# Optimization experiments

Hardware: AMD Instinct MI355X
Metric: run time of the kernel (lower is better)

The kernel has to match this reference:

```python
import jax, jax.numpy as jnp
import numpy as np


def setup_inputs() -> dict:
    key = jax.random.key(0)
    k1, k2 = jax.random.split(key)
    inputs = jax.random.normal(k1, (4, 128, 64, 64), dtype=jnp.float32)
    # binary hole mask (1 = known background, 0 = hole), broadcast over channels
    mask = jnp.round(jax.random.uniform(k2, (4, 1, 64, 64), dtype=jnp.float32))
    return {"inputs": inputs, "mask": mask}


def reference(inputs, mask):
    # SFFA contextual attention with 1x1 dynamic kernels.
    # Note: in the original torch code the 1x1 conv with padding=1 produces
    # border scores that conv_transpose2d with padding=1 crops away exactly,
    # so the math reduces to per-pixel matmul + softmax + matmul.
    bz, nc, h, w = inputs.shape
    N = h * w
    background = inputs * mask                              # [b, c, h, w]
    # dynamic kernels: one nc-dim vector per background pixel (patch)
    K = background.reshape(bz, nc, N).transpose(0, 2, 1) + 1e-7   # [b, N, c]
    Kn = K / jnp.sqrt(jnp.sum(K * K, axis=2, keepdims=True))      # l2-normalized
    feat = inputs.reshape(bz, nc, N)                        # [b, c, N]
    scores = jnp.einsum('bpc,bcn->bpn', Kn, feat)           # [b, N(patch), N(pixel)]
    attn = jax.nn.softmax(scores, axis=1)                   # softmax over patches p
    agg = jnp.einsum('bpc,bpn->bcn', K, attn).reshape(bz, nc, h, w)
    return background + agg * (1.0 - mask)
```

## Files before the change

### kernel.cpp

```cpp
#include <hip/hip_runtime.h>
#include <hip/hip_bf16.h>

typedef __attribute__((ext_vector_type(8))) short bf16x8;
typedef __attribute__((ext_vector_type(4))) float f32x4;

#define NPIX 4096
#define NC   128
#define RS128 0.08838834764831845f
#define KSP  6

#define GL2LDS(g, l) __builtin_amdgcn_global_load_lds( \
    (const __attribute__((address_space(1))) void*)(g), \
    (__attribute__((address_space(3))) void*)(l), 16, 0, 0)

__global__ __launch_bounds__(1024) void sffa_prep(
    const float* __restrict__ x, const float* __restrict__ mask,
    ushort* __restrict__ KnW, ushort* __restrict__ QW, ushort* __restrict__ VtW,
    float* __restrict__ s0c, int* __restrict__ pixQ, int* __restrict__ cnts,
    float* __restrict__ out)
{
    __shared__ float xs[128][69];
    __shared__ float ms[64];
    __shared__ float rinv[64];
    __shared__ float ssum[64];
    __shared__ float2 part[16][64];
    __shared__ int se[64];
    __shared__ int bgn[64];
    __shared__ int tinfo[2];
    __shared__ int wredP[16], wredT[16];
    const int tid = threadIdx.x;
    const int b = blockIdx.x >> 6, nblk = blockIdx.x & 63;
    const int n0 = nblk * 64;
    const float* xb = x + (size_t)b * NC * NPIX;
    float* ob = out + (size_t)b * NC * NPIX;

    #pragma unroll
    for (int it = 0; it < 2; ++it) {
        int e4 = it * 1024 + tid;
        int c = e4 >> 4, n4 = (e4 & 15) * 4;
        float4 v = *(const float4*)(xb + (size_t)c * NPIX + n0 + n4);
        xs[c][n4+0] = v.x; xs[c][n4+1] = v.y; xs[c][n4+2] = v.z; xs[c][n4+3] = v.w;
        *(float4*)(ob + (size_t)c * NPIX + n0 + n4) = v;
    }
    if (tid < 16) {
        float4 mv = *(const float4*)(mask + (size_t)b * NPIX + n0 + tid * 4);
        ms[tid*4+0] = mv.x; ms[tid*4+1] = mv.y; ms[tid*4+2] = mv.z; ms[tid*4+3] = mv.w;
    }
    {
        const int lane = tid & 63, w = tid >> 6;
        float4 mv = *(const float4*)(mask + (size_t)b * NPIX + tid * 4);
        int f0 = mv.x < 0.5f ? 0x10000 : 1;
        int f1 = mv.y < 0.5f ? 0x10000 : 1;
        int f2 = mv.z < 0.5f ? 0x10000 : 1;
        int f3 = mv.w < 0.5f ? 0x10000 : 1;
        int p0 = tid * 4;
        int pre = 0, tot = f0 + f1 + f2 + f3;
        if (p0 + 0 < n0) pre += f0;
        if (p0 + 1 < n0) pre += f1;
        if (p0 + 2 < n0) pre += f2;
        if (p0 + 3 < n0) pre += f3;
        #pragma unroll
        for (int d = 1; d < 64; d <<= 1) {
            pre += __shfl_xor(pre, d);
            tot += __shfl_xor(tot, d);
        }
        if (lane == 0) { wredP[w] = pre; wredT[w] = tot; }
    }
    __syncthreads();
    if (tid < 64) {
        int vP = (tid < 16) ? wredP[tid] : 0;
        int vT = (tid < 16) ? wredT[tid] : 0;
        #pragma unroll
        for (int d = 1; d < 16; d <<= 1) {
            vP += __shfl_xor(vP, d);
            vT += __shfl_xor(vT, d);
        }
        int base  = __shfl(vP, 0);
        int total = __shfl(vT, 0);
        if (tid == 0 && nblk == 0) {
            cnts[b * 2]     = total & 0xffff;
            cnts[b * 2 + 1] = total >> 16;
        }
        int f = ms[tid] > 0.5f ? 1 : 0x10000;
        int s = f;
        #pragma unroll
        for (int d = 1; d < 64; d <<= 1) {
            int t = __shfl_up(s, d);
            if (tid >= d) s += t;
        }
        se[tid] = base + s - f;
    }
    __syncthreads();
    {
        int p = tid & 63, qd = tid >> 6;
        float m = ms[p];
        float s2 = 0.f, s1 = 0.f;
        #pragma unroll
        for (int i = 0; i < 8; ++i) {
            float xv = xs[qd*8 + i][p];
            float k = fmaf(xv, m, 1e-7f);
            s2 = fmaf(k, k, s2);
            s1 += xv;
        }
        part[qd][p] = make_float2(s2, s1);
    }
    __syncthreads();
    if (tid < 64) {
        float s2 = 0.f, s1 = 0.f;
        #pragma unroll
        for (int k = 0; k < 16; ++k) { float2 t = part[k][tid]; s2 += t.x; s1 += t.y; }
        rinv[tid] = rsqrtf(s2);
        ssum[tid] = s1 * RS128;
    }
    __syncthreads();
    #pragma unroll
    for (int it = 0; it < 4; ++it) {
        int e2 = it * 1024 + tid;
        int n = e2 >> 6, cp = (e2 & 63) * 2;
        int pe = se[n];
        float x0 = xs[cp][n], x1 = xs[cp+1][n];
        if (ms[n] > 0.5f) {
            int slot = pe & 0xffff;
            float k0 = x0 + 1e-7f, k1 = x1 + 1e-7f;
            float r = rinv[n];
            __hip_bfloat162 kn;
            kn.x = __float2bfloat16(k0 * r); kn.y = __float2bfloat16(k1 * r);
            *(__hip_bfloat162*)(KnW + ((size_t)b * NPIX + slot) * NC + cp) = kn;
        } else {
            int slot = pe >> 16;
            __hip_bfloat162 q;
            q.x = __float2bfloat16(x0); q.y = __float2bfloat16(x1);
            *(__hip_bfloat162*)(QW + ((size_t)b * NPIX + slot) * NC + cp) = q;
        }
    }
    if (tid < 64) {
        if (ms[tid] < 0.5f) {
            int slot = se[tid] >> 16;
            s0c [(size_t)b * NPIX + slot] = ssum[tid];
            pixQ[(size_t)b * NPIX + slot] = n0 + tid;
        } else {
            bgn[(se[tid] & 0xffff) - (se[0] & 0xffff)] = tid;
        }
    }
    if (tid == 0) {
        tinfo[0] = se[0] & 0xffff;
        tinfo[1] = (se[63] & 0xffff) + (ms[63] > 0.5f ? 1 : 0) - (se[0] & 0xffff);
    }
    __syncthreads();
    {
        const int s0b = tinfo[0], nbg = tinfo[1];
        const int j = tid & 63, cg = tid >> 6;
        if (j < nbg) {
            int n = bgn[j];
            ushort* vcol = VtW + (size_t)b * NC * NPIX + s0b + j;
            #pragma unroll
            for (int cc = 0; cc < 8; ++cc) {
                int c = cg * 8 + cc;
                __hip_bfloat16 h = __float2bfloat16(xs[c][n] + 1e-7f);
                vcol[(size_t)c * NPIX] = *(ushort*)&h;
            }
        }
    }
}

#define L_V   16384
#define L_P   32768
#define L_ML  43008
#define L_SZ  44032

__global__ __launch_bounds__(512, 6) void sffa_attn(
    const ushort* __restrict__ KnW, const ushort* __restrict__ QW,
    const ushort* __restrict__ VtW, const int* __restrict__ cnts,
    ushort* __restrict__ partW, float* __restrict__ mlW)
{
    __shared__ __align__(16) char smem[L_SZ];
    const int tid  = threadIdx.x;
    const int w = tid >> 6, lane = tid & 63;
    const int l15 = lane & 15, g = lane >> 4;
    const int bx = (int)blockIdx.x;
    const int per = 64 * KSP;
    const int b = bx / per;
    const int rem = bx - b * per;
    const int qblk = rem / KSP, ks = rem - (rem / KSP) * KSP;
    const int q0 = qblk * 64;
    const int cntK = cnts[b * 2], cntQ = cnts[b * 2 + 1];
    if (q0 >= cntQ) return;
    const int blk = (b * 64 + qblk) * KSP + ks;

    const int nk64 = (cntK + 63) >> 6;
    const int tpk  = (nk64 + KSP - 1) / KSP;
    const int t0   = ks * tpk;
    const int NTK  = min(t0 + tpk, nk64) - t0;

    if (NTK <= 0) {
        unsigned* pz = (unsigned*)(partW + (size_t)blk * 8192);
        #pragma unroll
        for (int i = 0; i < 8; ++i) pz[i * 512 + tid] = 0u;
        if (tid < 64)
            *(float2*)(mlW + ((size_t)blk * 64 + tid) * 2) = make_float2(-1e30f, 0.f);
        return;
    }

    const int half = w >> 2;
    const int wq   = w & 3;
    const int kbase = t0 * 64;

    const ushort* Knb = KnW + (size_t)b * NPIX * NC;
    const ushort* Vtb = VtW + (size_t)b * NC * NPIX;

    bf16x8 qf[4];
    {
        const ushort* Qrow = QW + ((size_t)b * NPIX + q0 + wq * 16 + l15) * NC;
        #pragma unroll
        for (int kc = 0; kc < 4; ++kc)
            qf[kc] = *(const bf16x8*)(Qrow + 32 * kc + 8 * g);
    }

    const int rK = tid >> 4;
    const char* srcK = (const char*)(Knb + (size_t)(kbase + rK) * NC)
                     + (((tid & 15) ^ (rK & 15)) << 4);
    const int rV = tid >> 3;
    const char* srcV = (const char*)(Vtb + (size_t)rV * NPIX + kbase)
                     + (((tid & 7) ^ (rV & 7)) << 4);
    char* d0 = smem + tid * 16;

    GL2LDS(srcK,        d0);
    GL2LDS(srcK + 8192, d0 + 8192);
    GL2LDS(srcV,                           d0 + 16384);
    GL2LDS(srcV + (size_t)64 * NPIX * 2,   d0 + 24576);
    __syncthreads();

    f32x4 acc[8];
    const f32x4 fzero = {0.f, 0.f, 0.f, 0.f};
    #pragma unroll
    for (int i = 0; i < 8; ++i) acc[i] = fzero;
    float mrun = -1e30f, lrun = 0.f;
    char* Pw = smem + L_P + w * 1280;

    for (int kt = 0; kt < NTK; ++kt) {
        f32x4 sa0 = fzero, sa1 = fzero;
        {
            const char* rb0 = smem + (half * 32 + l15) * 256;
            const char* rb1 = rb0 + 4096;
            const int sw = l15 << 4;
            __builtin_amdgcn_s_setprio(1);
            #pragma unroll
            for (int kc = 0; kc < 4; ++kc) {
                int off = (64 * kc + 16 * g) ^ sw;
                bf16x8 a0 = *(const bf16x8*)(rb0 + off);
                bf16x8 a1 = *(const bf16x8*)(rb1 + off);
                sa0 = __builtin_amdgcn_mfma_f32_16x16x32_bf16(a0, qf[kc], sa0, 0, 0, 0);
                sa1 = __builtin_amdgcn_mfma_f32_16x16x32_bf16(a1, qf[kc], sa1, 0, 0, 0);
            }
            __builtin_amdgcn_s_setprio(0);
        }
        {
            int kg0 = (t0 + kt) * 64;
            if (kg0 + 64 > cntK) {
                int kb = cntK - kg0;
                int kr = half * 32 + 4 * g;
                #pragma unroll
                for (int r = 0; r < 4; ++r) {
                    if (kr + r >= kb)      sa0[r] = -3e38f;
                    if (kr + 16 + r >= kb) sa1[r] = -3e38f;
                }
            }
        }
        float tmax = fmaxf(fmaxf(fmaxf(sa0[0], sa0[1]), fmaxf(sa0[2], sa0[3])),
                           fmaxf(fmaxf(sa1[0], sa1[1]), fmaxf(sa1[2], sa1[3])));
        tmax = fmaxf(tmax, __shfl_xor(tmax, 16));
        tmax = fmaxf(tmax, __shfl_xor(tmax, 32));
        bool grow = !__all(tmax <= mrun + 8.f);
        float mnew = grow ? fmaxf(mrun, tmax) : mrun;
        float p0[4], p1[4];
        float ts = 0.f;
        #pragma unroll
        for (int r = 0; r < 4; ++r) { p0[r] = __expf(sa0[r] - mnew); ts += p0[r]; }
        #pragma unroll
        for (int r = 0; r < 4; ++r) { p1[r] = __expf(sa1[r] - mnew); ts += p1[r]; }
        ts += __shfl_xor(ts, 16);
        ts += __shfl_xor(ts, 32);
        if (grow) {
            float sc = __expf(mrun - mnew);
            lrun = lrun * sc + ts;
            float scr[4];
            #pragma unroll
            for (int r = 0; r < 4; ++r) scr[r] = __shfl(sc, 4 * g + r);
            #pragma unroll
            for (int ct = 0; ct < 8; ++ct) {
                acc[ct][0] *= scr[0]; acc[ct][1] *= scr[1];
                acc[ct][2] *= scr[2]; acc[ct][3] *= scr[3];
            }
            mrun = mnew;
        } else {
            lrun += ts;
        }
        union { __hip_bfloat162 h; unsigned u; } ua0, ua1, ub0, ub1;
        ua0.h.x = __float2bfloat16(p0[0]); ua0.h.y = __float2bfloat16(p0[1]);
        ua1.h.x = __float2bfloat16(p0[2]); ua1.h.y = __float2bfloat16(p0[3]);
        ub0.h.x = __float2bfloat16(p1[0]); ub0.h.y = __float2bfloat16(p1[1]);
        ub1.h.x = __float2bfloat16(p1[2]); ub1.h.y = __float2bfloat16(p1[3]);
        *(int2*)(Pw + l15 * 80 +      8 * g) = make_int2((int)ua0.u, (int)ua1.u);
        *(int2*)(Pw + l15 * 80 + 32 + 8 * g) = make_int2((int)ub0.u, (int)ub1.u);
        bf16x8 pf = *(const bf16x8*)(Pw + l15 * 80 + 16 * g);
        {
            const char* vb = smem + L_V;
            __builtin_amdgcn_s_setprio(1);
            #pragma unroll
            for (int ct = 0; ct < 8; ++ct) {
                int c = 16 * ct + l15;
                bf16x8 vf = *(const bf16x8*)(vb + c * 128 +
                                             ((64 * half + 16 * g) ^ ((c & 7) << 4)));
                acc[ct] = __builtin_amdgcn_mfma_f32_16x16x32_bf16(pf, vf, acc[ct], 0, 0, 0);
            }
            __builtin_amdgcn_s_setprio(0);
        }
        __syncthreads();
        if (kt + 1 < NTK) {
            const char* sK = srcK + (size_t)(kt + 1) * 16384;
            const char* sV = srcV + (size_t)(kt + 1) * 128;
            GL2LDS(sK,        d0);
            GL2LDS(sK + 8192, d0 + 8192);
            GL2LDS(sV,                         d0 + 16384);
            GL2LDS(sV + (size_t)64 * NPIX * 2, d0 + 24576);
            __syncthreads();
        }
    }

    float* ma = (float*)(smem + L_ML);
    float* la = ma + 64; float* mb = la + 64; float* lb = mb + 64;
    const int q = wq * 16 + l15;
    if (g == 0) {
        if (half == 0) { ma[q] = mrun; la[q] = lrun; }
        else           { mb[q] = mrun; lb[q] = lrun; }
    }
    __syncthreads();
    float* agg = (float*)smem;
    {
        float mstar = fmaxf(ma[q], mb[q]);
        float f = __expf(mrun - mstar);
        float fr[4];
        #pragma unroll
        for (int r = 0; r < 4; ++r) fr[r] = __shfl(f, 4 * g + r);
        if (half == 1) {
            #pragma unroll
            for (int ct = 0; ct < 8; ++ct) {
                int c = 16 * ct + l15;
                #pragma unroll
                for (int r = 0; r < 4; ++r)
                    agg[c * 68 + wq * 16 + 4 * g + r] = acc[ct][r] * fr[r];
            }
        }
        __syncthreads();
        if (half == 0) {
            #pragma unroll
            for (int ct = 0; ct < 8; ++ct) {
                int c = 16 * ct + l15;
                #pragma unroll
                for (int r = 0; r < 4; ++r) {
                    int idx = c * 68 + wq * 16 + 4 * g + r;
                    agg[idx] = acc[ct][r] * fr[r] + agg[idx];
                }
            }
        }
    }
    __syncthreads();
    if (tid < 64) {
        float M = fmaxf(ma[tid], mb[tid]);
        float ls = la[tid] * __expf(ma[tid] - M) + lb[tid] * __expf(mb[tid] - M);
        *(float2*)(mlW + ((size_t)blk * 64 + tid) * 2) = make_float2(M, ls);
    }
    ushort* pdst = partW + (size_t)blk * 8192;
    #pragma unroll
    for (int it = 0; it < 8; ++it) {
        int idx = it * 512 + tid;
        int c = idx >> 5, n2 = (idx & 31) * 2;
        __hip_bfloat162 h;
        h.x = __float2bfloat16(agg[c * 68 + n2]);
        h.y = __float2bfloat16(agg[c * 68 + n2 + 1]);
        *(__hip_bfloat162*)(pdst + c * 64 + n2) = h;
    }
}

__global__ __launch_bounds__(256) void sffa_comb(
    const ushort* __restrict__ partW, const float* __restrict__ mlW,
    const float* __restrict__ s0c, const int* __restrict__ pixQ,
    const int* __restrict__ cnts, float* __restrict__ out)
{
    __shared__ float wgtL[KSP][64];
    __shared__ int pixnL[64];
    const int tid = threadIdx.x;
    const int bx = blockIdx.x;
    const int b = bx >> 7, qb = (bx >> 1) & 63, ch = bx & 1;
    const int cntK = cnts[b * 2], cntQ = cnts[b * 2 + 1];
    if (qb * 64 >= cntQ) return;
    const int blkbase = (b * 64 + qb) * KSP;
    const float m0f = (float)(NPIX - cntK);

    if (tid < 64) {
        int slot = qb * 64 + tid;
        int pix = -1;
        if (slot < cntQ) {
            pix = pixQ[(size_t)b * NPIX + slot];
            float s0 = s0c[(size_t)b * NPIX + slot];
            float M = s0;
            float2 mls[KSP];
            #pragma unroll
            for (int k = 0; k < KSP; ++k) {
                mls[k] = *(const float2*)(mlW + ((size_t)(blkbase + k) * 64 + tid) * 2);
                M = fmaxf(M, mls[k].x);
            }
            float L = m0f * __expf(s0 - M);
            #pragma unroll
            for (int k = 0; k < KSP; ++k) L += mls[k].y * __expf(mls[k].x - M);
            float Li = 1.f / L;
            #pragma unroll
            for (int k = 0; k < KSP; ++k)
                wgtL[k][tid] = __expf(mls[k].x - M) * Li;
        }
        pixnL[tid] = pix;
    }
    __syncthreads();

    float* ob = out + ((size_t)b * NC + ch * 64) * NPIX;
    const ushort* pb = partW + (size_t)blkbase * 8192 + ch * 4096;
    #pragma unroll
    for (int it = 0; it < 2; ++it) {
        int idx = it * 256 + tid;
        int c = idx >> 3, grp = idx & 7;
        float v[8] = {0.f,0.f,0.f,0.f,0.f,0.f,0.f,0.f};
        #pragma unroll
        for (int k = 0; k < KSP; ++k) {
            ushort u[8];
            *(int4*)u = *(const int4*)(pb + (size_t)k * 8192 + c * 64 + grp * 8);
            #pragma unroll
            for (int j = 0; j < 8; ++j)
                v[j] = fmaf(__uint_as_float((unsigned)u[j] << 16),
                            wgtL[k][grp * 8 + j], v[j]);
        }
        #pragma unroll
        for (int j = 0; j < 8; ++j) {
            int pix = pixnL[grp * 8 + j];
            if (pix >= 0) ob[(size_t)c * NPIX + pix] = v[j];
        }
    }
}

extern "C" void kernel_launch(void* const* d_in, const int* in_sizes, int n_in,
                              void* d_out, int out_size, void* d_ws, size_t ws_size,
                              hipStream_t stream) {
    const float* x    = (const float*)d_in[0];
    const float* mask = (const float*)d_in[1];
    char* ws = (char*)d_ws;
    const size_t MBy = 1024 * 1024;
    const size_t KBy = 1024;

    ushort* KnW = (ushort*)(ws);
    ushort* QW  = (ushort*)(ws + 4 * MBy);
    ushort* VtW = (ushort*)(ws + 8 * MBy);

    ushort* partW = (ushort*)(ws + 12 * MBy);
    char* tail = ws + 12 * MBy + (size_t)(4 * 64 * KSP) * 16 * KBy;
    float* mlW  = (float*)(tail);
    float* s0c  = (float*)(tail + 1024 * KBy);
    int*   pixQ = (int*)(tail + 1088 * KBy);
    int*   cnts = (int*)(tail + 1152 * KBy);

    sffa_prep <<<256, 1024, 0, stream>>>(x, mask, KnW, QW, VtW, s0c, pixQ, cnts,
                                         (float*)d_out);
    sffa_attn <<<4 * 64 * KSP, 512, 0, stream>>>(KnW, QW, VtW, cnts, partW, mlW);
    sffa_comb <<<4 * 128, 256, 0, stream>>>(partW, mlW, s0c, pixQ, cnts,
                                            (float*)d_out);
}
```

Measured before the change: 64.39 us.

## Double query tile per block, double-buffer K/V loads, and raise key split

The attention kernel now processes 128 queries per block, two 16-row subtiles per wave, so each K/V tile staged in LDS is reused twice. K/V loads are double-buffered, with the next tile issued before computing the current one, which removes one barrier per iteration. The key split rises from 6 to 8, and the combine kernel and workspace layout are resized to match. LDS per block roughly doubles and the occupancy hint drops to 4, which reduces the number of resident blocks and raises register pressure.

Result: slower. 104.4 us (+62.1%).

```diff
diff --git a/kernel.cpp b/kernel.cpp
--- a/kernel.cpp
+++ b/kernel.cpp
@@ -7,7 +7,7 @@
 #define NPIX 4096
 #define NC   128
 #define RS128 0.08838834764831845f
-#define KSP  6
+#define KSP  8
 
 #define GL2LDS(g, l) __builtin_amdgcn_global_load_lds( \
     (const __attribute__((address_space(1))) void*)(g), \
@@ -163,12 +163,12 @@
     }
 }
 
-#define L_V   16384
-#define L_P   32768
-#define L_ML  43008
-#define L_SZ  44032
-
-__global__ __launch_bounds__(512, 6) void sffa_attn(
+#define L_BUF 32768
+#define L_P   65536
+#define L_ML  75776
+#define L_SZ  77824
+
+__global__ __launch_bounds__(512, 4) void sffa_attn(
     const ushort* __restrict__ KnW, const ushort* __restrict__ QW,
     const ushort* __restrict__ VtW, const int* __restrict__ cnts,
     ushort* __restrict__ partW, float* __restrict__ mlW)
@@ -178,14 +178,12 @@
     const int w = tid >> 6, lane = tid & 63;
     const int l15 = lane & 15, g = lane >> 4;
     const int bx = (int)blockIdx.x;
-    const int per = 64 * KSP;
-    const int b = bx / per;
-    const int rem = bx - b * per;
-    const int qblk = rem / KSP, ks = rem - (rem / KSP) * KSP;
-    const int q0 = qblk * 64;
+    const int b = bx >> 8, rem = bx & 255;
+    const int qblk = rem >> 3, ks = rem & 7;
+    const int q0 = qblk * 128;
     const int cntK = cnts[b * 2], cntQ = cnts[b * 2 + 1];
     if (q0 >= cntQ) return;
-    const int blk = (b * 64 + qblk) * KSP + ks;
+    const int blk = (b * 32 + qblk) * KSP + ks;
 
     const int nk64 = (cntK + 63) >> 6;
     const int tpk  = (nk64 + KSP - 1) / KSP;
@@ -193,11 +191,12 @@
     const int NTK  = min(t0 + tpk, nk64) - t0;
 
     if (NTK <= 0) {
-        unsigned* pz = (unsigned*)(partW + (size_t)blk * 8192);
-        #pragma unroll
-        for (int i = 0; i < 8; ++i) pz[i * 512 + tid] = 0u;
-        if (tid < 64)
-            *(float2*)(mlW + ((size_t)blk * 64 + tid) * 2) = make_float2(-1e30f, 0.f);
+        int4 z = {0,0,0,0};
+        int4* pz = (int4*)(partW + (size_t)blk * 16384);
+        #pragma unroll
+        for (int i = 0; i < 4; ++i) pz[i * 512 + tid] = z;
+        if (tid < 128)
+            *(float2*)(mlW + ((size_t)blk * 128 + tid) * 2) = make_float2(-1e30f, 0.f);
         return;
     }
 
@@ -208,12 +207,13 @@
     const ushort* Knb = KnW + (size_t)b * NPIX * NC;
     const ushort* Vtb = VtW + (size_t)b * NC * NPIX;
 
-    bf16x8 qf[4];
-    {
-        const ushort* Qrow = QW + ((size_t)b * NPIX + q0 + wq * 16 + l15) * NC;
+    bf16x8 qf[2][4];
+    #pragma unroll
+    for (int s = 0; s < 2; ++s) {
+        const ushort* Qrow = QW + ((size_t)b * NPIX + q0 + (wq + 4*s) * 16 + l15) * NC;
         #pragma unroll
         for (int kc = 0; kc < 4; ++kc)
-            qf[kc] = *(const bf16x8*)(Qrow + 32 * kc + 8 * g);
+            qf[s][kc] = *(const bf16x8*)(Qrow + 32 * kc + 8 * g);
     }
 
     const int rK = tid >> 4;
@@ -230,17 +230,30 @@
     GL2LDS(srcV + (size_t)64 * NPIX * 2,   d0 + 24576);
     __syncthreads();
 
-    f32x4 acc[8];
+    f32x4 acc[2][8];
     const f32x4 fzero = {0.f, 0.f, 0.f, 0.f};
     #pragma unroll
-    for (int i = 0; i < 8; ++i) acc[i] = fzero;
-    float mrun = -1e30f, lrun = 0.f;
+    for (int s = 0; s < 2; ++s)
+        #pragma unroll
+        for (int i = 0; i < 8; ++i) acc[s][i] = fzero;
+    float mrun[2] = {-1e30f, -1e30f}, lrun[2] = {0.f, 0.f};
     char* Pw = smem + L_P + w * 1280;
 
     for (int kt = 0; kt < NTK; ++kt) {
-        f32x4 sa0 = fzero, sa1 = fzero;
+        if (kt + 1 < NTK) {
+            char* nb = smem + ((kt + 1) & 1) * L_BUF + tid * 16;
+            const char* sK = srcK + (size_t)(kt + 1) * 16384;
+            const char* sV = srcV + (size_t)(kt + 1) * 128;
+            GL2LDS(sK,        nb);
+            GL2LDS(sK + 8192, nb + 8192);
+            GL2LDS(sV,                         nb + 16384);
+            GL2LDS(sV + (size_t)64 * NPIX * 2, nb + 24576);
+        }
+        char* bb = smem + (kt & 1) * L_BUF;
+        f32x4 sa[2][2];
+        sa[0][0] = fzero; sa[0][1] = fzero; sa[1][0] = fzero; sa[1][1] = fzero;
         {
-            const char* rb0 = smem + (half * 32 + l15) * 256;
+            const char* rb0 = bb + (half * 32 + l15) * 256;
             const char* rb1 = rb0 + 4096;
             const int sw = l15 << 4;
             __builtin_amdgcn_s_setprio(1);
@@ -249,8 +262,11 @@
                 int off = (64 * kc + 16 * g) ^ sw;
                 bf16x8 a0 = *(const bf16x8*)(rb0 + off);
                 bf16x8 a1 = *(const bf16x8*)(rb1 + off);
-                sa0 = __builtin_amdgcn_mfma_f32_16x16x32_bf16(a0, qf[kc], sa0, 0, 0, 0);
-                sa1 = __builtin_amdgcn_mfma_f32_16x16x32_bf16(a1, qf[kc], sa1, 0, 0, 0);
+                #pragma unroll
+                for (int s = 0; s < 2; ++s) {
+                    sa[s][0] = __builtin_amdgcn_mfma_f32_16x16x32_bf16(a0, qf[s][kc], sa[s][0], 0, 0, 0);
+                    sa[s][1] = __builtin_amdgcn_mfma_f32_16x16x32_bf16(a1, qf[s][kc], sa[s][1], 0, 0, 0);
+                }
             }
             __builtin_amdgcn_s_setprio(0);
         }
@@ -260,125 +276,133 @@
                 int kb = cntK - kg0;
                 int kr = half * 32 + 4 * g;
                 #pragma unroll
-                for (int r = 0; r < 4; ++r) {
-                    if (kr + r >= kb)      sa0[r] = -3e38f;
-                    if (kr + 16 + r >= kb) sa1[r] = -3e38f;
+                for (int s = 0; s < 2; ++s)
+                    #pragma unroll
+                    for (int r = 0; r < 4; ++r) {
+                        if (kr + r >= kb)      sa[s][0][r] = -3e38f;
+                        if (kr + 16 + r >= kb) sa[s][1][r] = -3e38f;
+                    }
+            }
+        }
+        #pragma unroll
+        for (int s = 0; s < 2; ++s) {
+            f32x4 sa0 = sa[s][0], sa1 = sa[s][1];
+            float tmax = fmaxf(fmaxf(fmaxf(sa0[0], sa0[1]), fmaxf(sa0[2], sa0[3])),
+                               fmaxf(fmaxf(sa1[0], sa1[1]), fmaxf(sa1[2], sa1[3])));
+            tmax = fmaxf(tmax, __shfl_xor(tmax, 16));
+            tmax = fmaxf(tmax, __shfl_xor(tmax, 32));
+            bool grow = !__all(tmax <= mrun[s] + 8.f);
+            float mnew = grow ? fmaxf(mrun[s], tmax) : mrun[s];
+            float p0[4], p1[4];
+            float ts = 0.f;
+            #pragma unroll
+            for (int r = 0; r < 4; ++r) { p0[r] = __expf(sa0[r] - mnew); ts += p0[r]; }
+            #pragma unroll
+            for (int r = 0; r < 4; ++r) { p1[r] = __expf(sa1[r] - mnew); ts += p1[r]; }
+            ts += __shfl_xor(ts, 16);
+            ts += __shfl_xor(ts, 32);
+            if (grow) {
+                float sc = __expf(mrun[s] - mnew);
+                lrun[s] = lrun[s] * sc + ts;
+                float scr[4];
+                #pragma unroll
+                for (int r = 0; r < 4; ++r) scr[r] = __shfl(sc, 4 * g + r);
+                #pragma unroll
+                for (int ct = 0; ct < 8; ++ct) {
+                    acc[s][ct][0] *= scr[0]; acc[s][ct][1] *= scr[1];
+                    acc[s][ct][2] *= scr[2]; acc[s][ct][3] *= scr[3];
                 }
-            }
-        }
-        float tmax = fmaxf(fmaxf(fmaxf(sa0[0], sa0[1]), fmaxf(sa0[2], sa0[3])),
-                           fmaxf(fmaxf(sa1[0], sa1[1]), fmaxf(sa1[2], sa1[3])));
-        tmax = fmaxf(tmax, __shfl_xor(tmax, 16));
-        tmax = fmaxf(tmax, __shfl_xor(tmax, 32));
-        bool grow = !__all(tmax <= mrun + 8.f);
-        float mnew = grow ? fmaxf(mrun, tmax) : mrun;
-        float p0[4], p1[4];
-        float ts = 0.f;
-        #pragma unroll
-        for (int r = 0; r < 4; ++r) { p0[r] = __expf(sa0[r] - mnew); ts += p0[r]; }
-        #pragma unroll
-        for (int r = 0; r < 4; ++r) { p1[r] = __expf(sa1[r] - mnew); ts += p1[r]; }
-        ts += __shfl_xor(ts, 16);
-        ts += __shfl_xor(ts, 32);
-        if (grow) {
-            float sc = __expf(mrun - mnew);
-            lrun = lrun * sc + ts;
-            float scr[4];
-            #pragma unroll
-            for (int r = 0; r < 4; ++r) scr[r] = __shfl(sc, 4 * g + r);
-            #pragma unroll
-            for (int ct = 0; ct < 8; ++ct) {
-                acc[ct][0] *= scr[0]; acc[ct][1] *= scr[1];
-                acc[ct][2] *= scr[2]; acc[ct][3] *= scr[3];
-            }
-            mrun = mnew;
-        } else {
-            lrun += ts;
-        }
-        union { __hip_bfloat162 h; unsigned u; } ua0, ua1, ub0, ub1;
-        ua0.h.x = __float2bfloat16(p0[0]); ua0.h.y = __float2bfloat16(p0[1]);
-        ua1.h.x = __float2bfloat16(p0[2]); ua1.h.y = __float2bfloat16(p0[3]);
-        ub0.h.x = __float2bfloat16(p1[0]); ub0.h.y = __float2bfloat16(p1[1]);
-        ub1.h.x = __float2bfloat16(p1[2]); ub1.h.y = __float2bfloat16(p1[3]);
-        *(int2*)(Pw + l15 * 80 +      8 * g) = make_int2((int)ua0.u, (int)ua1.u);
-        *(int2*)(Pw + l15 * 80 + 32 + 8 * g) = make_int2((int)ub0.u, (int)ub1.u);
-        bf16x8 pf = *(const bf16x8*)(Pw + l15 * 80 + 16 * g);
-        {
-            const char* vb = smem + L_V;
-            __builtin_amdgcn_s_setprio(1);
-            #pragma unroll
-            for (int ct = 0; ct < 8; ++ct) {
-                int c = 16 * ct + l15;
-                bf16x8 vf = *(const bf16x8*)(vb + c * 128 +
-                                             ((64 * half + 16 * g) ^ ((c & 7) << 4)));
-                acc[ct] = __builtin_amdgcn_mfma_f32_16x16x32_bf16(pf, vf, acc[ct], 0, 0, 0);
-            }
-            __builtin_amdgcn_s_setprio(0);
+                mrun[s] = mnew;
+            } else {
+                lrun[s] += ts;
+            }
+            union { __hip_bfloat162 h; unsigned u; } ua0, ua1, ub0, ub1;
+            ua0.h.x = __float2bfloat16(p0[0]); ua0.h.y = __float2bfloat16(p0[1]);
+            ua1.h.x = __float2bfloat16(p0[2]); ua1.h.y = __float2bfloat16(p0[3]);
+            ub0.h.x = __float2bfloat16(p1[0]); ub0.h.y = __float2bfloat16(p1[1]);
+            ub1.h.x = __float2bfloat16(p1[2]); ub1.h.y = __float2bfloat16(p1[3]);
+            *(int2*)(Pw + l15 * 80 +      8 * g) = make_int2((int)ua0.u, (int)ua1.u);
+            *(int2*)(Pw + l15 * 80 + 32 + 8 * g) = make_int2((int)ub0.u, (int)ub1.u);
+            bf16x8 pf = *(const bf16x8*)(Pw + l15 * 80 + 16 * g);
+            {
+                const char* vb = bb + 16384;
+                __builtin_amdgcn_s_setprio(1);
+                #pragma unroll
+                for (int ct = 0; ct < 8; ++ct) {
+                    int c = 16 * ct + l15;
+                    bf16x8 vf = *(const bf16x8*)(vb + c * 128 +
+                                                 ((64 * half + 16 * g) ^ ((c & 7) << 4)));
+                    acc[s][ct] = __builtin_amdgcn_mfma_f32_16x16x32_bf16(pf, vf, acc[s][ct], 0, 0, 0);
+                }
+                __builtin_amdgcn_s_setprio(0);
+            }
         }
         __syncthreads();
-        if (kt + 1 < NTK) {
-            const char* sK = srcK + (size_t)(kt + 1) * 16384;
-            const char* sV = srcV + (size_t)(kt + 1) * 128;
-            GL2LDS(sK,        d0);
-            GL2LDS(sK + 8192, d0 + 8192);
-            GL2LDS(sV,                         d0 + 16384);
-            GL2LDS(sV + (size_t)64 * NPIX * 2, d0 + 24576);
-            __syncthreads();
-        }
     }
 
     float* ma = (float*)(smem + L_ML);
-    float* la = ma + 64; float* mb = la + 64; float* lb = mb + 64;
-    const int q = wq * 16 + l15;
-    if (g == 0) {
-        if (half == 0) { ma[q] = mrun; la[q] = lrun; }
-        else           { mb[q] = mrun; lb[q] = lrun; }
+    float* la = ma + 128; float* mb = la + 128; float* lb = mb + 128;
+    #pragma unroll
+    for (int s = 0; s < 2; ++s) {
+        int q = (wq + 4*s) * 16 + l15;
+        if (g == 0) {
+            if (half == 0) { ma[q] = mrun[s]; la[q] = lrun[s]; }
+            else           { mb[q] = mrun[s]; lb[q] = lrun[s]; }
+        }
     }
     __syncthreads();
     float* agg = (float*)smem;
     {
-        float mstar = fmaxf(ma[q], mb[q]);
-        float f = __expf(mrun - mstar);
-        float fr[4];
-        #pragma unroll
-        for (int r = 0; r < 4; ++r) fr[r] = __shfl(f, 4 * g + r);
+        float fr[2][4];
+        #pragma unroll
+        for (int s = 0; s < 2; ++s) {
+            int q = (wq + 4*s) * 16 + l15;
+            float mstar = fmaxf(ma[q], mb[q]);
+            float f = __expf(mrun[s] - mstar);
+            #pragma unroll
+            for (int r = 0; r < 4; ++r) fr[s][r] = __shfl(f, 4 * g + r);
+        }
         if (half == 1) {
             #pragma unroll
-            for (int ct = 0; ct < 8; ++ct) {
-                int c = 16 * ct + l15;
-                #pragma unroll
-                for (int r = 0; r < 4; ++r)
-                    agg[c * 68 + wq * 16 + 4 * g + r] = acc[ct][r] * fr[r];
-            }
+            for (int s = 0; s < 2; ++s)
+                #pragma unroll
+                for (int ct = 0; ct < 8; ++ct) {
+                    int c = 16 * ct + l15;
+                    #pragma unroll
+                    for (int r = 0; r < 4; ++r)
+                        agg[c * 132 + (wq + 4*s) * 16 + 4 * g + r] = acc[s][ct][r] * fr[s][r];
+                }
         }
         __syncthreads();
         if (half == 0) {
             #pragma unroll
-            for (int ct = 0; ct < 8; ++ct) {
-                int c = 16 * ct + l15;
-                #pragma unroll
-                for (int r = 0; r < 4; ++r) {
-                    int idx = c * 68 + wq * 16 + 4 * g + r;
-                    agg[idx] = acc[ct][r] * fr[r] + agg[idx];
+            for (int s = 0; s < 2; ++s)
+                #pragma unroll
+                for (int ct = 0; ct < 8; ++ct) {
+                    int c = 16 * ct + l15;
+                    #pragma unroll
+                    for (int r = 0; r < 4; ++r) {
+                        int idx = c * 132 + (wq + 4*s) * 16 + 4 * g + r;
+                        agg[idx] = acc[s][ct][r] * fr[s][r] + agg[idx];
+                    }
                 }
-            }
-        }
-    }
-    __syncthreads();
-    if (tid < 64) {
+        }
+    }
+    __syncthreads();
+    if (tid < 128) {
         float M = fmaxf(ma[tid], mb[tid]);
         float ls = la[tid] * __expf(ma[tid] - M) + lb[tid] * __expf(mb[tid] - M);
-        *(float2*)(mlW + ((size_t)blk * 64 + tid) * 2) = make_float2(M, ls);
-    }
-    ushort* pdst = partW + (size_t)blk * 8192;
-    #pragma unroll
-    for (int it = 0; it < 8; ++it) {
+        *(float2*)(mlW + ((size_t)blk * 128 + tid) * 2) = make_float2(M, ls);
+    }
+    ushort* pdst = partW + (size_t)blk * 16384;
+    #pragma unroll
+    for (int it = 0; it < 16; ++it) {
         int idx = it * 512 + tid;
-        int c = idx >> 5, n2 = (idx & 31) * 2;
+        int c = idx >> 6, n2 = (idx & 63) * 2;
         __hip_bfloat162 h;
-        h.x = __float2bfloat16(agg[c * 68 + n2]);
-        h.y = __float2bfloat16(agg[c * 68 + n2 + 1]);
-        *(__hip_bfloat162*)(pdst + c * 64 + n2) = h;
+        h.x = __float2bfloat16(agg[c * 132 + n2]);
+        h.y = __float2bfloat16(agg[c * 132 + n2 + 1]);
+        *(__hip_bfloat162*)(pdst + c * 128 + n2) = h;
     }
 }
 
@@ -387,18 +411,18 @@
     const float* __restrict__ s0c, const int* __restrict__ pixQ,
     const int* __restrict__ cnts, float* __restrict__ out)
 {
-    __shared__ float wgtL[KSP][64];
-    __shared__ int pixnL[64];
+    __shared__ float wgtL[KSP][128];
+    __shared__ int pixnL[128];
     const int tid = threadIdx.x;
     const int bx = blockIdx.x;
-    const int b = bx >> 7, qb = (bx >> 1) & 63, ch = bx & 1;
+    const int b = bx >> 6, qb = (bx >> 1) & 31, ch = bx & 1;
     const int cntK = cnts[b * 2], cntQ = cnts[b * 2 + 1];
-    if (qb * 64 >= cntQ) return;
-    const int blkbase = (b * 64 + qb) * KSP;
+    if (qb * 128 >= cntQ) return;
+    const int blkbase = (b * 32 + qb) * KSP;
     const float m0f = (float)(NPIX - cntK);
 
-    if (tid < 64) {
-        int slot = qb * 64 + tid;
+    if (tid < 128) {
+        int slot = qb * 128 + tid;
         int pix = -1;
         if (slot < cntQ) {
             pix = pixQ[(size_t)b * NPIX + slot];
@@ -407,7 +431,7 @@
             float2 mls[KSP];
             #pragma unroll
             for (int k = 0; k < KSP; ++k) {
-                mls[k] = *(const float2*)(mlW + ((size_t)(blkbase + k) * 64 + tid) * 2);
+                mls[k] = *(const float2*)(mlW + ((size_t)(blkbase + k) * 128 + tid) * 2);
                 M = fmaxf(M, mls[k].x);
             }
             float L = m0f * __expf(s0 - M);
@@ -422,17 +446,17 @@
     }
     __syncthreads();
 
-    float* ob = out + ((size_t)b * NC + ch * 64) * NPIX;
-    const ushort* pb = partW + (size_t)blkbase * 8192 + ch * 4096;
-    #pragma unroll
-    for (int it = 0; it < 2; ++it) {
+    float* ob = out + (size_t)b * NC * NPIX;
+    const ushort* pb = partW + (size_t)blkbase * 16384;
+    #pragma unroll
+    for (int it = 0; it < 4; ++it) {
         int idx = it * 256 + tid;
-        int c = idx >> 3, grp = idx & 7;
+        int c = ch * 64 + (idx >> 4), grp = idx & 15;
         float v[8] = {0.f,0.f,0.f,0.f,0.f,0.f,0.f,0.f};
         #pragma unroll
         for (int k = 0; k < KSP; ++k) {
             ushort u[8];
-            *(int4*)u = *(const int4*)(pb + (size_t)k * 8192 + c * 64 + grp * 8);
+            *(int4*)u = *(const int4*)(pb + (size_t)k * 16384 + c * 128 + grp * 8);
             #pragma unroll
             for (int j = 0; j < 8; ++j)
                 v[j] = fmaf(__uint_as_float((unsigned)u[j] << 16),
@@ -460,7 +484,7 @@
     ushort* VtW = (ushort*)(ws + 8 * MBy);
 
     ushort* partW = (ushort*)(ws + 12 * MBy);
-    char* tail = ws + 12 * MBy + (size_t)(4 * 64 * KSP) * 16 * KBy;
+    char* tail = ws + 44 * MBy;
     float* mlW  = (float*)(tail);
     float* s0c  = (float*)(tail + 1024 * KBy);
     int*   pixQ = (int*)(tail + 1088 * KBy);
@@ -468,7 +492,7 @@
 
     sffa_prep <<<256, 1024, 0, stream>>>(x, mask, KnW, QW, VtW, s0c, pixQ, cnts,
                                          (float*)d_out);
-    sffa_attn <<<4 * 64 * KSP, 512, 0, stream>>>(KnW, QW, VtW, cnts, partW, mlW);
-    sffa_comb <<<4 * 128, 256, 0, stream>>>(partW, mlW, s0c, pixQ, cnts,
-                                            (float*)d_out);
+    sffa_attn <<<4 * 32 * KSP, 512, 0, stream>>>(KnW, QW, VtW, cnts, partW, mlW);
+    sffa_comb <<<4 * 32 * 2, 256, 0, stream>>>(partW, mlW, s0c, pixQ, cnts,
+                                               (float*)d_out);
 }
```
